# Performance work log

Measured on AMD Instinct MI355X. Metric: run time of the kernel, lower is better.

## Reference

```python
import jax, jax.numpy as jnp
import numpy as np

C, H, N, B, L = 1, 512, 64, 16, 2048  # n_channels, n_heads, d_kernel, batch, seq_len


def setup_inputs() -> dict:
    key = jax.random.key(0)
    k1, k2 = jax.random.split(key)
    u = jax.random.normal(k1, (B, C * H, L), dtype=jnp.float32)
    k = jax.random.normal(k2, (C, H, N), dtype=jnp.float32)
    return {"u": u, "k": k}


def _l1_normalize(x, axis):
    # torch.linalg.norm(x, ord=1, dim=axis, keepdim=True): vector 1-norm along `axis`
    return x / jnp.sum(jnp.abs(x), axis=axis, keepdims=True)


def _forward(u, k):
    c, h, n = k.shape
    bsz, d, l = u.shape  # d == c*h
    dt = u.dtype
    # Shift matrix A: A[:, :, 1:, :-1] = I  (companion-style shift)
    A = jnp.zeros((c, h, n, n), dtype=dt).at[:, :, 1:, :-1].set(jnp.eye(n - 1, dtype=dt))
    # b = e1 broadcast to (c, h, n)
    b_vec = jnp.zeros((c, h, n), dtype=dt).at[:, :, 0].set(1.0)
    # closed-loop: k_norm = L1-normalize(clamp(k, 1/16, 1)); A_cl = L1-normalize(A + b k^T)
    k_norm = _l1_normalize(jnp.clip(k, 1.0 / 16.0, 1.0), axis=2)
    BK = jnp.einsum('chi,chj->chij', b_vec, k_norm)
    M = _l1_normalize(A + BK, axis=2)

    # Krylov recurrence: f[i] = k . (M^i b), i = 0..l-1
    def step(x, _):
        f_i = jnp.einsum('chn,chn->ch', k, x)
        x_next = jnp.einsum('chij,chj->chi', M, x)
        return x_next, f_i

    _, f = jax.lax.scan(step, b_vec, None, length=l)  # f: (l, c, h)
    f = jnp.moveaxis(f, 0, -1)  # (c, h, l)

    # Causal FFT convolution of u (b, c, h, l) with filter f (c, h, l)
    n_fft = 2 * l
    uf = jnp.fft.rfft(u.reshape(bsz, c, h, l), n=n_fft)
    ff = jnp.fft.rfft(f, n=n_fft)
    y = jnp.fft.irfft(uf * ff[None], n=n_fft)[..., :l]
    return y.reshape(bsz, c * h, l)


def reference(u, k):
    return _forward(u, k)
```

## Files before the change

kernel.cpp:

```cpp
#include <hip/hip_runtime.h>


namespace {

constexpr int kH = 512;
constexpr int kL = 2048;
constexpr int kChunks = 32;

typedef __attribute__((ext_vector_type(8))) short bf16x8;
typedef __attribute__((ext_vector_type(4))) float f32x4;

#define MFMA(A, B, C) __builtin_amdgcn_mfma_f32_16x16x32_bf16((A), (B), (C), 0, 0, 0)

__device__ inline unsigned int cvt_pk_bf16(float lo, float hi) {
  unsigned int r;
  asm("v_cvt_pk_bf16_f32 %0, %1, %2" : "=v"(r) : "v"(lo), "v"(hi));
  return r;
}

union B8U4 { bf16x8 v; unsigned int u[4]; };

__device__ inline void cvt_split8(const f32x4 a, const f32x4 b, bf16x8& fh, bf16x8& fl) {
  B8U4 H, L;
  float x[8];
  #pragma unroll
  for (int j = 0; j < 4; ++j) { x[j] = a[j]; x[4 + j] = b[j]; }
  #pragma unroll
  for (int d = 0; d < 4; ++d) {
    const float x0 = x[2 * d], x1 = x[2 * d + 1];
    const unsigned int hp = cvt_pk_bf16(x0, x1);
    const float h0 = __uint_as_float(hp << 16);
    const float h1 = __uint_as_float(hp & 0xFFFF0000u);
    H.u[d] = hp;
    L.u[d] = cvt_pk_bf16(x0 - h0, x1 - h1);
  }
  fh = H.v; fl = L.v;
}

__device__ inline void gen_frag(const float* tp, int n0, bf16x8& fh, bf16x8& fl) {
  float t[8];
  #pragma unroll
  for (int j = 0; j < 8; ++j) {
    const int n = n0 - j;
    t[j] = (n >= 0 && n < 127) ? tp[n] : 0.0f;
  }
  const f32x4 a = {t[0], t[1], t[2], t[3]};
  const f32x4 b = {t[4], t[5], t[6], t[7]};
  cvt_split8(a, b, fh, fl);
}

__device__ inline void gen_fragB(const float* tp, int base, bf16x8& fh, bf16x8& fl) {
  float t[8];
  #pragma unroll
  for (int j = 0; j < 8; ++j) t[j] = tp[base + j];
  const f32x4 a = {t[0], t[1], t[2], t[3]};
  const f32x4 b = {t[4], t[5], t[6], t[7]};
  cvt_split8(a, b, fh, fl);
}


__global__ __launch_bounds__(128, 1)
void ssm_mfma_kernel(const float* __restrict__ u,
                     const float* __restrict__ kin,
                     float* __restrict__ y) {
  const int h    = blockIdx.x;
  const int tid  = threadIdx.x;
  const int wid  = tid >> 6;
  const int lane = tid & 63;
  const int ln16 = lane & 15;
  const int quad = lane >> 4;

  __shared__ alignas(16) char pool[36864];
  auto Astage  = (float (*)[68]) (pool);
  auto Pstage  = (float (*)[68]) (pool + 17408);
  auto cring   = (float (*)[16][68]) (pool);
  auto yuring  = (float (*)[16][68]) (pool + 8704);
  auto scratch = (float (*)[68]) (pool + 17408);
  auto taps    = (float (*)[128]) (pool + 34816);
  float* wPad  = (float*) (pool + 36352);

  if (wid == 0) {
    const float kv = kin[h * 64 + lane];
    const float kc = fminf(fmaxf(kv, 0.0625f), 1.0f);
    float ks = kc;
    #pragma unroll
    for (int off = 32; off >= 1; off >>= 1) ks += __shfl_xor(ks, off);
    const float kn = kc / ks;
    const float cc = 1.0f / (1.0f + kn);
    float pp = cc;
    #pragma unroll
    for (int off = 1; off < 64; off <<= 1) {
      const float t = __shfl_up(pp, off);
      if (lane >= off) pp *= t;
    }
    float Pe = __shfl_up(pp, 1);
    if (lane == 0) Pe = 1.0f;
    const float wv = (lane < 63) ? (kn * cc * Pe) : Pe;
    const float gv = kv * Pe;
    float sv = (lane == 0) ? 1.0f : 0.0f;
    for (int rr = 0; rr < 63; ++rr) {
      const float s0 = __shfl(sv, rr);
      const float cf = __shfl(wv, lane - 1 - rr);
      if (lane > rr) sv = fmaf(cf, s0, sv);
    }
    taps[0][lane] = 0.0f;
    taps[1][lane] = 0.0f;
    const float gn = __shfl(gv, lane + 1);
    taps[2][lane] = (lane < 63) ? gn : 0.0f;
    taps[2][64 + lane] = 0.0f;
    taps[0][63 + lane] = sv;
    taps[1][63 + lane] = gv;
    if (lane == 0) { taps[0][127] = 0.0f; taps[1][127] = 0.0f; }
    wPad[lane] = wv;
    wPad[64 + lane] = 0.0f;
  }
  __syncthreads();

  #pragma unroll
  for (int t2 = 0; t2 < 2; ++t2) {
    const int mt = 2 * wid + t2;
    bf16x8 xh[2], xl[2], g2h[2], g2l[2];
    #pragma unroll
    for (int tk = 0; tk < 2; ++tk) {
      const int n0 = 16 * mt + ln16 - (32 * tk + 8 * quad) + 63;
      gen_frag(taps[0], n0, xh[tk], xl[tk]);
      gen_frag(taps[1], n0, g2h[tk], g2l[tk]);
    }
    #pragma unroll
    for (int nt = 0; nt < 4; ++nt) {
      f32x4 accA = {0.f, 0.f, 0.f, 0.f};
      f32x4 accG = {0.f, 0.f, 0.f, 0.f};
      #pragma unroll
      for (int tk = 0; tk < 2; ++tk) {
        const int base = 8 * quad + 32 * tk - (16 * nt + ln16) + 63;
        bf16x8 bh, bl;
        gen_fragB(wPad, base, bh, bl);
        accA = MFMA(xh[tk], bh, accA);
        accA = MFMA(xh[tk], bl, accA);
        accA = MFMA(xl[tk], bh, accA);
        accA = MFMA(xl[tk], bl, accA);
        bf16x8 sbh, sbl;
        gen_fragB(taps[0], base, sbh, sbl);
        accG = MFMA(g2h[tk], sbh, accG);
        accG = MFMA(g2h[tk], sbl, accG);
        accG = MFMA(g2l[tk], sbh, accG);
      }
      #pragma unroll
      for (int r = 0; r < 4; ++r) {
        Astage[16 * mt + 4 * quad + r][16 * nt + ln16] = accA[r];
        Pstage[16 * mt + 4 * quad + r][16 * nt + ln16] = accG[r];
      }
    }
  }
  __syncthreads();

  bf16x8 oxH[4][2], oxL[4][2], oyH[4][2], oyL[4][2];
  if (wid == 1) {
    #pragma unroll
    for (int mt = 0; mt < 4; ++mt) {
      #pragma unroll
      for (int tk = 0; tk < 2; ++tk) {
        const int n0 = 16 * mt + ln16 - (32 * tk + 8 * quad) + 63;
        gen_frag(taps[0], n0, oxH[mt][tk], oxL[mt][tk]);
        const int row = 16 * mt + ln16, k0 = 32 * tk + 8 * quad;
        const f32x4 a = *(const f32x4*)&Pstage[row][k0];
        const f32x4 b = *(const f32x4*)&Pstage[row][k0 + 4];
        cvt_split8(a, b, oyH[mt][tk], oyL[mt][tk]);
      }
    }
  }
  __syncthreads();

  #pragma unroll
  for (int t2 = 0; t2 < 2; ++t2) {
    const int mt = 2 * wid + t2;
    bf16x8 g2h[2], g2l[2];
    #pragma unroll
    for (int tk = 0; tk < 2; ++tk) {
      const int n0 = 16 * mt + ln16 - (32 * tk + 8 * quad) + 63;
      gen_frag(taps[1], n0, g2h[tk], g2l[tk]);
    }
    #pragma unroll
    for (int nt = 0; nt < 4; ++nt) {
      f32x4 acc = {0.f, 0.f, 0.f, 0.f};
      #pragma unroll
      for (int tk = 0; tk < 2; ++tk) {
        float t[8];
        #pragma unroll
        for (int j = 0; j < 8; ++j)
          t[j] = Astage[8 * quad + 32 * tk + j][16 * nt + ln16];
        const f32x4 a = {t[0], t[1], t[2], t[3]};
        const f32x4 b = {t[4], t[5], t[6], t[7]};
        bf16x8 bh, bl;
        cvt_split8(a, b, bh, bl);
        acc = MFMA(g2h[tk], bh, acc);
        acc = MFMA(g2h[tk], bl, acc);
        acc = MFMA(g2l[tk], bh, acc);
      }
      #pragma unroll
      for (int r = 0; r < 4; ++r) {
        const int i = 16 * mt + 4 * quad + r, j = 16 * nt + ln16;
        Pstage[i][j] = acc[r] + taps[2][(i - j) + 63];
      }
    }
  }
  __syncthreads();

  if (wid == 0) {
    #pragma unroll
    for (int mt = 0; mt < 4; ++mt) {
      #pragma unroll
      for (int tk = 0; tk < 2; ++tk) {
        const int row = 16 * mt + ln16, k0 = 32 * tk + 8 * quad;
        f32x4 a = *(const f32x4*)&Astage[row][k0];
        f32x4 b = *(const f32x4*)&Astage[row][k0 + 4];
        cvt_split8(a, b, oxH[mt][tk], oxL[mt][tk]);
        a = *(const f32x4*)&Pstage[row][k0];
        b = *(const f32x4*)&Pstage[row][k0 + 4];
        cvt_split8(a, b, oyH[mt][tk], oyL[mt][tk]);
      }
    }
  }
  __syncthreads();

  bf16x8 opH[2], opL[2];
  {
    bf16x8 z;
    #pragma unroll
    for (int j = 0; j < 8; ++j) z[j] = 0;
    opH[0] = z; opH[1] = z; opL[0] = z; opL[1] = z;
  }

  const float* ub = u + ((size_t)ln16 * kH + h) * kL + 8 * quad;
  float* yb = y + ((size_t)ln16 * kH + h) * kL;

  f32x4 uv[4];
  if (wid == 1) {
    #pragma unroll
    for (int i = 0; i < 4; ++i)
      uv[i] = *(const f32x4*)(ub + 32 * (i >> 1) + 4 * (i & 1));
  }

  #pragma unroll 1
  for (int s = 0; s <= kChunks; ++s) {
    if (wid == 1) {
      if (s < kChunks) {
        cvt_split8(uv[0], uv[1], opH[0], opL[0]);
        cvt_split8(uv[2], uv[3], opH[1], opL[1]);
        const int tn = (s + 1 < kChunks) ? 64 * (s + 1) : 0;
        #pragma unroll
        for (int i = 0; i < 4; ++i)
          uv[i] = *(const f32x4*)(ub + tn + 32 * (i >> 1) + 4 * (i & 1));
        const int par = s & 1;
        #pragma unroll
        for (int mt = 0; mt < 4; ++mt) {
          f32x4 aX = {0.f, 0.f, 0.f, 0.f};
          f32x4 aY = {0.f, 0.f, 0.f, 0.f};
          #pragma unroll
          for (int tk = 0; tk < 2; ++tk) {
            aX = MFMA(oxH[mt][tk], opH[tk], aX);
            aX = MFMA(oxH[mt][tk], opL[tk], aX);
            aX = MFMA(oxL[mt][tk], opH[tk], aX);
            aY = MFMA(oyH[mt][tk], opH[tk], aY);
            aY = MFMA(oyH[mt][tk], opL[tk], aY);
            aY = MFMA(oyL[mt][tk], opH[tk], aY);
          }
          *(f32x4*)&cring[par][ln16][16 * mt + 4 * quad] = aX;
          *(f32x4*)&yuring[par][ln16][16 * mt + 4 * quad] = aY;
        }
      }
    } else {
      if (s >= 1) {
        const int par = (s - 1) & 1;
        f32x4 aX[4], aY[4];
        #pragma unroll
        for (int mt = 0; mt < 4; ++mt) {
          aX[mt] = *(const f32x4*)&cring[par][ln16][16 * mt + 4 * quad];
          aY[mt] = *(const f32x4*)&yuring[par][ln16][16 * mt + 4 * quad];
        }
        #pragma unroll
        for (int mt = 0; mt < 4; ++mt) {
          #pragma unroll
          for (int tk = 0; tk < 2; ++tk) {
            aX[mt] = MFMA(oxH[mt][tk], opH[tk], aX[mt]);
            aX[mt] = MFMA(oxH[mt][tk], opL[tk], aX[mt]);
            aX[mt] = MFMA(oxL[mt][tk], opH[tk], aX[mt]);
            aY[mt] = MFMA(oyH[mt][tk], opH[tk], aY[mt]);
            aY[mt] = MFMA(oyH[mt][tk], opL[tk], aY[mt]);
            aY[mt] = MFMA(oyL[mt][tk], opH[tk], aY[mt]);
          }
        }
        #pragma unroll
        for (int mt = 0; mt < 4; ++mt) {
          *(f32x4*)&scratch[ln16][16 * mt + 4 * quad] = aX[mt];
          *(f32x4*)(yb + 64 * (s - 1) + 16 * mt + 4 * quad) = aY[mt];
        }
        asm volatile("s_waitcnt lgkmcnt(0)" ::: "memory");
        __builtin_amdgcn_sched_barrier(0);
        #pragma unroll
        for (int tk = 0; tk < 2; ++tk) {
          const int k0 = 8 * quad + 32 * tk;
          const f32x4 ra = *(const f32x4*)&scratch[ln16][k0];
          const f32x4 rb = *(const f32x4*)&scratch[ln16][k0 + 4];
          cvt_split8(ra, rb, opH[tk], opL[tk]);
        }
      }
    }
    asm volatile("s_waitcnt lgkmcnt(0)" ::: "memory");
    __builtin_amdgcn_s_barrier();
    asm volatile("" ::: "memory");
  }
}

}

extern "C" void kernel_launch(void* const* d_in, const int* in_sizes, int n_in,
                              void* d_out, int out_size, void* d_ws, size_t ws_size,
                              hipStream_t stream) {
  const float* u  = (const float*)d_in[0];
  const float* kk = (const float*)d_in[1];
  if (n_in >= 2 && in_sizes[0] < in_sizes[1]) {
    const float* t = u; u = kk; kk = t;
  }
  float* yy = (float*)d_out;
  hipLaunchKernelGGL(ssm_mfma_kernel, dim3(kH), dim3(128), 0, stream, u, kk, yy);
}
```

Before: 150.1 us.

## Split chunk scan across four waves with a three-stage ring pipeline

Grows the block from two to four wavefronts and gives each wave one matrix role: two waves compute the per-chunk input projections (state and output contributions), one wave runs the serial state-carry update, and one wave applies the output update and writes y. A three-deep LDS ring for the state lets the output wave lag the state wave by one chunk, which takes the output MFMAs off the serial critical path. The cost is one extra pipeline step, more barriers per block, and more LDS traffic.

```diff
diff --git a/kernel.cpp b/kernel.cpp
--- a/kernel.cpp
+++ b/kernel.cpp
@@ -59,7 +59,7 @@
 }
 
 
-__global__ __launch_bounds__(128, 1)
+__global__ __launch_bounds__(256, 1)
 void ssm_mfma_kernel(const float* __restrict__ u,
                      const float* __restrict__ kin,
                      float* __restrict__ y) {
@@ -73,9 +73,9 @@
   __shared__ alignas(16) char pool[36864];
   auto Astage  = (float (*)[68]) (pool);
   auto Pstage  = (float (*)[68]) (pool + 17408);
-  auto cring   = (float (*)[16][68]) (pool);
-  auto yuring  = (float (*)[16][68]) (pool + 8704);
-  auto scratch = (float (*)[68]) (pool + 17408);
+  auto sring   = (float (*)[16][68]) (pool);
+  auto cring   = (float (*)[16][68]) (pool + 13056);
+  auto yuring  = (float (*)[16][68]) (pool + 21760);
   auto taps    = (float (*)[128]) (pool + 34816);
   float* wPad  = (float*) (pool + 36352);
 
@@ -116,9 +116,8 @@
   }
   __syncthreads();
 
-  #pragma unroll
-  for (int t2 = 0; t2 < 2; ++t2) {
-    const int mt = 2 * wid + t2;
+  {
+    const int mt = wid;
     bf16x8 xh[2], xl[2], g2h[2], g2l[2];
     #pragma unroll
     for (int tk = 0; tk < 2; ++tk) {
@@ -154,26 +153,32 @@
   }
   __syncthreads();
 
-  bf16x8 oxH[4][2], oxL[4][2], oyH[4][2], oyL[4][2];
-  if (wid == 1) {
+  bf16x8 oxH[4][2], oxL[4][2];
+  if (wid == 2) {
     #pragma unroll
     for (int mt = 0; mt < 4; ++mt) {
       #pragma unroll
       for (int tk = 0; tk < 2; ++tk) {
         const int n0 = 16 * mt + ln16 - (32 * tk + 8 * quad) + 63;
         gen_frag(taps[0], n0, oxH[mt][tk], oxL[mt][tk]);
+      }
+    }
+  } else if (wid == 3) {
+    #pragma unroll
+    for (int mt = 0; mt < 4; ++mt) {
+      #pragma unroll
+      for (int tk = 0; tk < 2; ++tk) {
         const int row = 16 * mt + ln16, k0 = 32 * tk + 8 * quad;
         const f32x4 a = *(const f32x4*)&Pstage[row][k0];
         const f32x4 b = *(const f32x4*)&Pstage[row][k0 + 4];
-        cvt_split8(a, b, oyH[mt][tk], oyL[mt][tk]);
-      }
-    }
-  }
-  __syncthreads();
-
-  #pragma unroll
-  for (int t2 = 0; t2 < 2; ++t2) {
-    const int mt = 2 * wid + t2;
+        cvt_split8(a, b, oxH[mt][tk], oxL[mt][tk]);
+      }
+    }
+  }
+  __syncthreads();
+
+  {
+    const int mt = wid;
     bf16x8 g2h[2], g2l[2];
     #pragma unroll
     for (int tk = 0; tk < 2; ++tk) {
@@ -212,12 +217,20 @@
       #pragma unroll
       for (int tk = 0; tk < 2; ++tk) {
         const int row = 16 * mt + ln16, k0 = 32 * tk + 8 * quad;
-        f32x4 a = *(const f32x4*)&Astage[row][k0];
-        f32x4 b = *(const f32x4*)&Astage[row][k0 + 4];
+        const f32x4 a = *(const f32x4*)&Astage[row][k0];
+        const f32x4 b = *(const f32x4*)&Astage[row][k0 + 4];
         cvt_split8(a, b, oxH[mt][tk], oxL[mt][tk]);
-        a = *(const f32x4*)&Pstage[row][k0];
-        b = *(const f32x4*)&Pstage[row][k0 + 4];
-        cvt_split8(a, b, oyH[mt][tk], oyL[mt][tk]);
+      }
+    }
+  } else if (wid == 1) {
+    #pragma unroll
+    for (int mt = 0; mt < 4; ++mt) {
+      #pragma unroll
+      for (int tk = 0; tk < 2; ++tk) {
+        const int row = 16 * mt + ln16, k0 = 32 * tk + 8 * quad;
+        const f32x4 a = *(const f32x4*)&Pstage[row][k0];
+        const f32x4 b = *(const f32x4*)&Pstage[row][k0 + 4];
+        cvt_split8(a, b, oxH[mt][tk], oxL[mt][tk]);
       }
     }
   }
@@ -235,15 +248,18 @@
   float* yb = y + ((size_t)ln16 * kH + h) * kL;
 
   f32x4 uv[4];
-  if (wid == 1) {
+  if (wid >= 2) {
     #pragma unroll
     for (int i = 0; i < 4; ++i)
       uv[i] = *(const f32x4*)(ub + 32 * (i >> 1) + 4 * (i & 1));
   }
 
   #pragma unroll 1
-  for (int s = 0; s <= kChunks; ++s) {
-    if (wid == 1) {
+  for (int s = 0; s < kChunks + 2; ++s) {
+    const int m3  = s % 3;
+    const int m3a = (m3 == 2) ? 0 : m3 + 1;
+    const int m3b = (m3 == 0) ? 2 : m3 - 1;
+    if (wid >= 2) {
       if (s < kChunks) {
         cvt_split8(uv[0], uv[1], opH[0], opL[0]);
         cvt_split8(uv[2], uv[3], opH[1], opL[1]);
@@ -251,59 +267,76 @@
         #pragma unroll
         for (int i = 0; i < 4; ++i)
           uv[i] = *(const f32x4*)(ub + tn + 32 * (i >> 1) + 4 * (i & 1));
-        const int par = s & 1;
+        f32x4 acc[4] = {};
         #pragma unroll
         for (int mt = 0; mt < 4; ++mt) {
-          f32x4 aX = {0.f, 0.f, 0.f, 0.f};
-          f32x4 aY = {0.f, 0.f, 0.f, 0.f};
-          #pragma unroll
-          for (int tk = 0; tk < 2; ++tk) {
-            aX = MFMA(oxH[mt][tk], opH[tk], aX);
-            aX = MFMA(oxH[mt][tk], opL[tk], aX);
-            aX = MFMA(oxL[mt][tk], opH[tk], aX);
-            aY = MFMA(oyH[mt][tk], opH[tk], aY);
-            aY = MFMA(oyH[mt][tk], opL[tk], aY);
-            aY = MFMA(oyL[mt][tk], opH[tk], aY);
-          }
-          *(f32x4*)&cring[par][ln16][16 * mt + 4 * quad] = aX;
-          *(f32x4*)&yuring[par][ln16][16 * mt + 4 * quad] = aY;
-        }
+          #pragma unroll
+          for (int tk = 0; tk < 2; ++tk) {
+            acc[mt] = MFMA(oxH[mt][tk], opH[tk], acc[mt]);
+            acc[mt] = MFMA(oxH[mt][tk], opL[tk], acc[mt]);
+            acc[mt] = MFMA(oxL[mt][tk], opH[tk], acc[mt]);
+          }
+        }
+        float* dst = (wid == 2) ? &cring[s & 1][0][0] : &yuring[m3][0][0];
+        #pragma unroll
+        for (int mt = 0; mt < 4; ++mt)
+          *(f32x4*)&dst[ln16 * 68 + 16 * mt + 4 * quad] = acc[mt];
+      }
+    } else if (wid == 0) {
+      if (s >= 1 && s <= kChunks) {
+        if (s >= 2) {
+          #pragma unroll
+          for (int tk = 0; tk < 2; ++tk) {
+            const int k0 = 8 * quad + 32 * tk;
+            const f32x4 ra = *(const f32x4*)&sring[m3a][ln16][k0];
+            const f32x4 rb = *(const f32x4*)&sring[m3a][ln16][k0 + 4];
+            cvt_split8(ra, rb, opH[tk], opL[tk]);
+          }
+        }
+        f32x4 acc[4];
+        #pragma unroll
+        for (int mt = 0; mt < 4; ++mt)
+          acc[mt] = *(const f32x4*)&cring[(s - 1) & 1][ln16][16 * mt + 4 * quad];
+        #pragma unroll
+        for (int mt = 0; mt < 4; ++mt) {
+          #pragma unroll
+          for (int tk = 0; tk < 2; ++tk) {
+            acc[mt] = MFMA(oxH[mt][tk], opH[tk], acc[mt]);
+            acc[mt] = MFMA(oxH[mt][tk], opL[tk], acc[mt]);
+            acc[mt] = MFMA(oxL[mt][tk], opH[tk], acc[mt]);
+          }
+        }
+        #pragma unroll
+        for (int mt = 0; mt < 4; ++mt)
+          *(f32x4*)&sring[m3b][ln16][16 * mt + 4 * quad] = acc[mt];
       }
     } else {
-      if (s >= 1) {
-        const int par = (s - 1) & 1;
-        f32x4 aX[4], aY[4];
+      if (s >= 2) {
+        if (s >= 3) {
+          #pragma unroll
+          for (int tk = 0; tk < 2; ++tk) {
+            const int k0 = 8 * quad + 32 * tk;
+            const f32x4 ra = *(const f32x4*)&sring[m3][ln16][k0];
+            const f32x4 rb = *(const f32x4*)&sring[m3][ln16][k0 + 4];
+            cvt_split8(ra, rb, opH[tk], opL[tk]);
+          }
+        }
+        f32x4 acc[4];
+        #pragma unroll
+        for (int mt = 0; mt < 4; ++mt)
+          acc[mt] = *(const f32x4*)&yuring[m3a][ln16][16 * mt + 4 * quad];
         #pragma unroll
         for (int mt = 0; mt < 4; ++mt) {
-          aX[mt] = *(const f32x4*)&cring[par][ln16][16 * mt + 4 * quad];
-          aY[mt] = *(const f32x4*)&yuring[par][ln16][16 * mt + 4 * quad];
-        }
-        #pragma unroll
-        for (int mt = 0; mt < 4; ++mt) {
-          #pragma unroll
-          for (int tk = 0; tk < 2; ++tk) {
-            aX[mt] = MFMA(oxH[mt][tk], opH[tk], aX[mt]);
-            aX[mt] = MFMA(oxH[mt][tk], opL[tk], aX[mt]);
-            aX[mt] = MFMA(oxL[mt][tk], opH[tk], aX[mt]);
-            aY[mt] = MFMA(oyH[mt][tk], opH[tk], aY[mt]);
-            aY[mt] = MFMA(oyH[mt][tk], opL[tk], aY[mt]);
-            aY[mt] = MFMA(oyL[mt][tk], opH[tk], aY[mt]);
-          }
-        }
-        #pragma unroll
-        for (int mt = 0; mt < 4; ++mt) {
-          *(f32x4*)&scratch[ln16][16 * mt + 4 * quad] = aX[mt];
-          *(f32x4*)(yb + 64 * (s - 1) + 16 * mt + 4 * quad) = aY[mt];
-        }
-        asm volatile("s_waitcnt lgkmcnt(0)" ::: "memory");
-        __builtin_amdgcn_sched_barrier(0);
-        #pragma unroll
-        for (int tk = 0; tk < 2; ++tk) {
-          const int k0 = 8 * quad + 32 * tk;
-          const f32x4 ra = *(const f32x4*)&scratch[ln16][k0];
-          const f32x4 rb = *(const f32x4*)&scratch[ln16][k0 + 4];
-          cvt_split8(ra, rb, opH[tk], opL[tk]);
-        }
+          #pragma unroll
+          for (int tk = 0; tk < 2; ++tk) {
+            acc[mt] = MFMA(oxH[mt][tk], opH[tk], acc[mt]);
+            acc[mt] = MFMA(oxH[mt][tk], opL[tk], acc[mt]);
+            acc[mt] = MFMA(oxL[mt][tk], opH[tk], acc[mt]);
+          }
+        }
+        #pragma unroll
+        for (int mt = 0; mt < 4; ++mt)
+          *(f32x4*)(yb + 64 * (s - 2) + 16 * mt + 4 * quad) = acc[mt];
       }
     }
     asm volatile("s_waitcnt lgkmcnt(0)" ::: "memory");
@@ -323,5 +356,5 @@
     const float* t = u; u = kk; kk = t;
   }
   float* yy = (float*)d_out;
-  hipLaunchKernelGGL(ssm_mfma_kernel, dim3(kH), dim3(128), 0, stream, u, kk, yy);
-}
+  hipLaunchKernelGGL(ssm_mfma_kernel, dim3(kH), dim3(256), 0, stream, u, kk, yy);
+}
```

New measurement: 145.9 us. 2.8% less time.
